# Optimization experiments

Hardware: AMD Instinct MI355X
Metric: run time of the kernel (lower is better)

Reference implementation:

```python
import jax, jax.numpy as jnp
import numpy as np
import math

H = 16          # num heads
D = 64          # head dim
MAX_POS = 512   # max_position_embeddings


def setup_inputs() -> dict:
    key = jax.random.key(0)
    ks = jax.random.split(key, 8)
    B, S, E = 8, 512, 1024
    scale = 1.0 / math.sqrt(E)
    return {
        "hidden_states": jax.random.normal(ks[0], (B, S, E), jnp.float32),
        "attention_mask": jnp.zeros((B, 1, 1, S), jnp.float32),
        "Wq": jax.random.normal(ks[1], (E, E), jnp.float32) * scale,
        "bq": jnp.zeros((E,), jnp.float32),
        "Wk": jax.random.normal(ks[2], (E, E), jnp.float32) * scale,
        "bk": jnp.zeros((E,), jnp.float32),
        "Wv": jax.random.normal(ks[3], (E, E), jnp.float32) * scale,
        "bv": jnp.zeros((E,), jnp.float32),
        "dist_emb": jax.random.normal(ks[4], (2 * MAX_POS - 1, D), jnp.float32) * 0.02,
    }


def reference(hidden_states, attention_mask, Wq, bq, Wk, bk, Wv, bv, dist_emb):
    B, S, E = hidden_states.shape

    def heads(x):  # [B,S,E] -> [B,H,S,D]
        return x.reshape(B, S, H, D).transpose(0, 2, 1, 3)

    q = heads(hidden_states @ Wq + bq)
    k = heads(hidden_states @ Wk + bk)
    v = heads(hidden_states @ Wv + bv)

    # raw scores [B,H,S,S]
    scores = jnp.einsum('bhld,bhrd->bhlr', q, k)

    # relative position embedding lookup: distance[l,r] = l - r
    pos = jnp.arange(S)
    distance = pos[:, None] - pos[None, :]               # [S,S]
    pe = dist_emb[distance + MAX_POS - 1]                # [S,S,D]
    scores = scores + jnp.einsum('bhld,lrd->bhlr', q, pe)
    scores = scores + jnp.einsum('bhrd,lrd->bhlr', k, pe)

    scores = scores / math.sqrt(D) + attention_mask
    probs = jax.nn.softmax(scores, axis=-1)

    ctx = jnp.einsum('bhlr,bhrd->bhld', probs, v)        # [B,H,S,D]
    ctx = ctx.transpose(0, 2, 1, 3).reshape(B, S, H * D)
    return ctx
```

## Files before the change

kernel.cpp:

```cpp
#include <hip/hip_runtime.h>

#define BATCH 8
#define SEQ   512
#define EMB   1024
#define NH    16
#define HD    64

typedef __bf16 bf16x8 __attribute__((ext_vector_type(8)));
typedef float  f32x4  __attribute__((ext_vector_type(4)));

__device__ __forceinline__ unsigned short f2bf(float f){
  union { float f; unsigned u; } v; v.f = f;
  unsigned r = v.u + 0x7FFFu + ((v.u >> 16) & 1u);
  return (unsigned short)(r >> 16);
}
__device__ __forceinline__ unsigned short f2bfr(float f){
  union { float f; unsigned u; } v; v.f = f;
  return (unsigned short)((v.u + 0x8000u) >> 16);
}
__device__ __forceinline__ float bf2f(unsigned short s){
  union { unsigned u; float f; } v; v.u = ((unsigned)s) << 16;
  return v.f;
}

__device__ __forceinline__ float dpp_max16(float x){
  int t;
  t = __builtin_amdgcn_update_dpp(0, __builtin_bit_cast(int, x), 0xB1, 0xF, 0xF, true);
  x = fmaxf(x, __builtin_bit_cast(float, t));
  t = __builtin_amdgcn_update_dpp(0, __builtin_bit_cast(int, x), 0x4E, 0xF, 0xF, true);
  x = fmaxf(x, __builtin_bit_cast(float, t));
  t = __builtin_amdgcn_update_dpp(0, __builtin_bit_cast(int, x), 0x141, 0xF, 0xF, true);
  x = fmaxf(x, __builtin_bit_cast(float, t));
  t = __builtin_amdgcn_update_dpp(0, __builtin_bit_cast(int, x), 0x140, 0xF, 0xF, true);
  x = fmaxf(x, __builtin_bit_cast(float, t));
  return x;
}
__device__ __forceinline__ float dpp_sum16(float x){
  int t;
  t = __builtin_amdgcn_update_dpp(0, __builtin_bit_cast(int, x), 0xB1, 0xF, 0xF, true);
  x += __builtin_bit_cast(float, t);
  t = __builtin_amdgcn_update_dpp(0, __builtin_bit_cast(int, x), 0x4E, 0xF, 0xF, true);
  x += __builtin_bit_cast(float, t);
  t = __builtin_amdgcn_update_dpp(0, __builtin_bit_cast(int, x), 0x141, 0xF, 0xF, true);
  x += __builtin_bit_cast(float, t);
  t = __builtin_amdgcn_update_dpp(0, __builtin_bit_cast(int, x), 0x140, 0xF, 0xF, true);
  x += __builtin_bit_cast(float, t);
  return x;
}

__device__ __forceinline__ int swzc(int row, int chunk){
  return row * 128 + (((chunk ^ (row & 7)) & 7) << 4);
}
__device__ __forceinline__ int swz2(int row, int col){
  return row * 128 + ((((col >> 3) ^ (row & 7)) & 7) << 4) + ((col & 7) << 1);
}

__device__ __forceinline__ void gload16(const unsigned short* g, unsigned char* lds){
  __builtin_amdgcn_global_load_lds((const __attribute__((address_space(1))) unsigned int*)g,
                                   (__attribute__((address_space(3))) unsigned int*)lds,
                                   16, 0, 0);
}

__device__ __forceinline__ void bar_lds(){
  asm volatile("s_waitcnt lgkmcnt(0)" ::: "memory");
  __builtin_amdgcn_s_barrier();
}

__global__ void k_pre(const float* __restrict__ hid, unsigned short* __restrict__ hidb,
                      const float* __restrict__ dist, unsigned short* __restrict__ distb,
                      const float* __restrict__ Wq, const float* __restrict__ Wk,
                      const float* __restrict__ Wv, unsigned short* __restrict__ wqt,
                      unsigned short* __restrict__ wkt, unsigned short* __restrict__ wvt){
  int bid = blockIdx.x;
  int t = threadIdx.x;
  if (bid < 4096){
    int i = (bid * 256 + t) * 4;
    float4 v = *(const float4*)(hid + i);
    ushort4 o; o.x = f2bf(v.x); o.y = f2bf(v.y); o.z = f2bf(v.z); o.w = f2bf(v.w);
    *(ushort4*)(hidb + i) = o;
  } else if (bid < 4352){
    int i = (bid - 4096) * 256 + t;
    distb[i] = (i < 1023 * 64) ? f2bf(dist[i]) : (unsigned short)0;
  } else {
    int wt = bid - 4352;
    int z = wt >> 10, rem = wt & 1023;
    const float* W = (z == 0) ? Wq : (z == 1) ? Wk : Wv;
    unsigned short* WT = (z == 0) ? wqt : (z == 1) ? wkt : wvt;
    __shared__ float tl[32][33];
    int n0 = (rem & 31) * 32, k0 = (rem >> 5) * 32;
    int tx = t & 31, ty = t >> 5;
#pragma unroll
    for (int i = 0; i < 4; i++)
      tl[ty + 8*i][tx] = W[(k0 + ty + 8*i) * EMB + n0 + tx];
    __syncthreads();
#pragma unroll
    for (int i = 0; i < 4; i++)
      WT[(n0 + ty + 8*i) * EMB + k0 + tx] = f2bf(tl[tx][ty + 8*i]);
  }
}

__global__ __launch_bounds__(256, 3) void k_gemm3(const unsigned short* __restrict__ A,
                                                  const unsigned short* __restrict__ wqt,
                                                  const unsigned short* __restrict__ wkt,
                                                  const unsigned short* __restrict__ wvt,
                                                  const float* __restrict__ bq,
                                                  const float* __restrict__ bk,
                                                  const float* __restrict__ bv,
                                                  unsigned short* __restrict__ qb,
                                                  unsigned short* __restrict__ kb,
                                                  unsigned short* __restrict__ vtb){
  int z = blockIdx.z;
  const unsigned short* BT = (z == 0) ? wqt : (z == 1) ? wkt : wvt;
  const float* bias = (z == 0) ? bq : (z == 1) ? bk : bv;
  unsigned short* out = (z == 0) ? qb : (z == 1) ? kb : vtb;
  int mode = (z == 2);

  __shared__ __align__(16) unsigned char sA[128 * 128];
  __shared__ __align__(16) unsigned char sB[128 * 128];
  int id2 = blockIdx.x + 8 * blockIdx.y;
  int s2  = (id2 & 7) * 32 + (id2 >> 3);
  int m0 = (s2 >> 3) * 128, n0 = (s2 & 7) * 128;
  int t = threadIdx.x, w = t >> 6, lane = t & 63, g = lane >> 4, lr = lane & 15;
  int rowbase = (w >> 1) * 64, colbase = (w & 1) * 64;
  int lrow = lane >> 3, lc = lane & 7;
  f32x4 acc[4][4] = {};
  for (int k0 = 0; k0 < EMB; k0 += 64){
    __syncthreads();
#pragma unroll
    for (int i = 0; i < 4; i++){
      int row = (w + 4*i) * 8 + lrow;
      int cg  = lc ^ (row & 7);
      gload16(A  + (m0 + row) * EMB + k0 + cg*8, sA + (w + 4*i) * 1024);
      gload16(BT + (n0 + row) * EMB + k0 + cg*8, sB + (w + 4*i) * 1024);
    }
    __syncthreads();
#pragma unroll
    for (int kk = 0; kk < 2; kk++){
      bf16x8 af[4], bfv[4];
#pragma unroll
      for (int i = 0; i < 4; i++) af[i]  = *(const bf16x8*)(sA + swzc(rowbase + 16*i + lr, kk*4 + g));
#pragma unroll
      for (int j = 0; j < 4; j++) bfv[j] = *(const bf16x8*)(sB + swzc(colbase + 16*j + lr, kk*4 + g));
#pragma unroll
      for (int i = 0; i < 4; i++)
#pragma unroll
        for (int j = 0; j < 4; j++)
          acc[i][j] = __builtin_amdgcn_mfma_f32_16x16x32_bf16(af[i], bfv[j], acc[i][j], 0, 0, 0);
    }
  }
#pragma unroll
  for (int i = 0; i < 4; i++)
#pragma unroll
    for (int j = 0; j < 4; j++)
#pragma unroll
      for (int r = 0; r < 4; r++){
        int m = m0 + rowbase + 16*i + 4*g + r;
        int n = n0 + colbase + 16*j + lr;
        float val = acc[i][j][r] + bias[n];
        int b = m >> 9, s = m & 511, h = n >> 6, d = n & 63;
        int idx = (mode == 0) ? (((b*NH + h)*SEQ + s)*HD + d)
                              : (((b*NH + h)*HD + d)*SEQ + s);
        out[idx] = f2bf(val);
      }
}

__global__ __launch_bounds__(256, 2) void k_attn(const unsigned short* __restrict__ qb,
                                                 const unsigned short* __restrict__ kb,
                                                 const unsigned short* __restrict__ vtb,
                                                 const unsigned short* __restrict__ distb,
                                                 const float* __restrict__ mask,
                                                 float* __restrict__ out){
  __shared__ __align__(16) unsigned char sK[64 * 128];
  __shared__ __align__(16) unsigned char sV[64 * 128];
  __shared__ __align__(16) unsigned char sSA[4][2624];
  __shared__ __align__(16) unsigned char sSB[4][2560];

  const float SCL  = 0.125f * 1.4426950408889634f;
  const float L2E  = 1.4426950408889634f;

  int bid = blockIdx.x;
  int wgid = (bid & 7) * 128 + (bid >> 3);
  int lt = wgid & 7, h = (wgid >> 3) & 15, b = wgid >> 7;
  int L0 = lt * 64;
  int bh = b * NH + h;
  int t = threadIdx.x, w = t >> 6, lane = t & 63, g = lane >> 4, lr = lane & 15;
  int lbase = 16 * w;
  unsigned char* mySA = sSA[w];
  unsigned char* mySB = sSB[w];
  unsigned char* myP  = mySA;
  const float* maskp = mask + b * SEQ;

  const unsigned short* qrow = qb + (bh * SEQ + L0 + lbase + lr) * HD + 8 * g;
  bf16x8 aq0 = *(const bf16x8*)qrow;
  bf16x8 aq1 = *(const bf16x8*)(qrow + 32);

  bf16x8 pe[5][2];
#define LOAD_PE(JB) do {                                                     \
    const unsigned short* _pb = distb + ((JB) + 16*w + lr) * HD + 8*g;       \
    _Pragma("unroll")                                                        \
    for (int _j = 0; _j < 5; _j++){                                          \
      pe[_j][0] = *(const bf16x8*)(_pb + _j*16*HD);                          \
      pe[_j][1] = *(const bf16x8*)(_pb + _j*16*HD + 32); }                   \
  } while(0)

  int lrow = lane >> 3, lc = lane & 7;
  int row0 = w * 8 + lrow,      row1 = (w + 4) * 8 + lrow;
  int cg0  = lc ^ (row0 & 7),   cg1  = lc ^ (row1 & 7);
  const unsigned short* kbase = kb  + bh * SEQ * HD;
  const unsigned short* vbase = vtb + bh * HD * SEQ;

  uint4 kst0 = *(const uint4*)(kbase + row0 * HD  + cg0 * 8);
  uint4 kst1 = *(const uint4*)(kbase + row1 * HD  + cg1 * 8);
  uint4 vst0 = *(const uint4*)(vbase + row0 * SEQ + cg0 * 8);
  uint4 vst1 = *(const uint4*)(vbase + row1 * SEQ + cg1 * 8);
  LOAD_PE(L0 + 448);

  f32x4 o[4] = {};
  float mrun[4], srun[4];
#pragma unroll
  for (int r = 0; r < 4; r++){ mrun[r] = -1e30f; srun[r] = 0.f; }

  for (int rt = 0; rt < 8; rt++){
    int R0 = rt * 64;

    bar_lds();

    *(uint4*)(sK + w * 1024 + lane * 16)       = kst0;
    *(uint4*)(sK + (w + 4) * 1024 + lane * 16) = kst1;
    *(uint4*)(sV + w * 1024 + lane * 16)       = vst0;
    *(uint4*)(sV + (w + 4) * 1024 + lane * 16) = vst1;

    if (rt < 7){
      const unsigned short* ks = kbase + (R0 + 64) * HD;
      const unsigned short* vs = vbase + (R0 + 64);
      kst0 = *(const uint4*)(ks + row0 * HD  + cg0 * 8);
      kst1 = *(const uint4*)(ks + row1 * HD  + cg1 * 8);
      vst0 = *(const uint4*)(vs + row0 * SEQ + cg0 * 8);
      vst1 = *(const uint4*)(vs + row1 * SEQ + cg1 * 8);
    }

    float mreg[4];
#pragma unroll
    for (int f = 0; f < 4; f++) mreg[f] = maskp[R0 + 16*f + lr];

    bar_lds();

    __builtin_amdgcn_s_setprio(1);
    f32x4 sc[4];
#pragma unroll
    for (int f = 0; f < 4; f++){
      bf16x8 k0 = *(const bf16x8*)(sK + swzc(16*f + lr, g));
      bf16x8 k1 = *(const bf16x8*)(sK + swzc(16*f + lr, 4 + g));
      f32x4 a = {};
      a = __builtin_amdgcn_mfma_f32_16x16x32_bf16(aq0, k0, a, 0, 0, 0);
      a = __builtin_amdgcn_mfma_f32_16x16x32_bf16(aq1, k1, a, 0, 0, 0);
      sc[f] = a;
      f32x4 b0 = {}, b1 = {};
      b0 = __builtin_amdgcn_mfma_f32_16x16x32_bf16(k0, pe[3 - f][0], b0, 0, 0, 0);
      b0 = __builtin_amdgcn_mfma_f32_16x16x32_bf16(k1, pe[3 - f][1], b0, 0, 0, 0);
      b1 = __builtin_amdgcn_mfma_f32_16x16x32_bf16(k0, pe[4 - f][0], b1, 0, 0, 0);
      b1 = __builtin_amdgcn_mfma_f32_16x16x32_bf16(k1, pe[4 - f][1], b1, 0, 0, 0);
#pragma unroll
      for (int reg = 0; reg < 4; reg++){
        int ss = 4*g + reg + lr;
        float v = (ss >= 15) ? b0[reg] : b1[reg];
        int row = 16*f + 4*g + reg;
        int col = (ss + 1) & 15;
        *(unsigned short*)(mySB + row*40 + col*2) = f2bfr(v);
      }
    }

#pragma unroll
    for (int jt2 = 0; jt2 < 5; jt2++){
      f32x4 a = {};
      a = __builtin_amdgcn_mfma_f32_16x16x32_bf16(aq0, pe[jt2][0], a, 0, 0, 0);
      a = __builtin_amdgcn_mfma_f32_16x16x32_bf16(aq1, pe[jt2][1], a, 0, 0, 0);
#pragma unroll
      for (int reg = 0; reg < 4; reg++){
        int rloc = 63 + 4*g + reg - lr - 16*jt2;
        int addr = ((unsigned)rloc < 64u) ? (rloc*40 + (4*g + reg)*2) : 2560;
        *(unsigned short*)(mySA + addr) = f2bfr(a[reg]);
      }
    }
    __builtin_amdgcn_s_setprio(0);

    if (rt < 7) LOAD_PE(L0 + 448 - 64*(rt + 1));

#pragma unroll
    for (int f = 0; f < 4; f++){
      ushort4 sa = *(const ushort4*)(mySA + (16*f + lr)*40 + 8*g);
      ushort4 sb = *(const ushort4*)(mySB + (16*f + lr)*40 + 8*g);
      float madd = mreg[f] * L2E;
      sc[f][0] = (sc[f][0] + bf2f(sa.x) + bf2f(sb.x)) * SCL + madd;
      sc[f][1] = (sc[f][1] + bf2f(sa.y) + bf2f(sb.y)) * SCL + madd;
      sc[f][2] = (sc[f][2] + bf2f(sa.z) + bf2f(sb.z)) * SCL + madd;
      sc[f][3] = (sc[f][3] + bf2f(sa.w) + bf2f(sb.w)) * SCL + madd;
    }

    float fac[4];
#pragma unroll
    for (int r = 0; r < 4; r++){
      float tm = fmaxf(fmaxf(sc[0][r], sc[1][r]), fmaxf(sc[2][r], sc[3][r]));
      tm = dpp_max16(tm);
      float mnew = fmaxf(mrun[r], tm);
      float fr = exp2f(mrun[r] - mnew);
      float ps = 0.f;
#pragma unroll
      for (int f = 0; f < 4; f++){ float p = exp2f(sc[f][r] - mnew); sc[f][r] = p; ps += p; }
      ps = dpp_sum16(ps);
      srun[r] = srun[r] * fr + ps;
      mrun[r] = mnew;
      fac[r]  = fr;
    }
#pragma unroll
    for (int df = 0; df < 4; df++)
#pragma unroll
      for (int r = 0; r < 4; r++) o[df][r] *= fac[r];

#pragma unroll
    for (int f = 0; f < 4; f++)
#pragma unroll
      for (int r = 0; r < 4; r++)
        *(unsigned short*)(myP + swz2(4*g + r, 16*f + lr)) = f2bfr(sc[f][r]);

    __builtin_amdgcn_s_setprio(1);
#pragma unroll
    for (int kk = 0; kk < 2; kk++){
      bf16x8 pf = *(const bf16x8*)(myP + swzc(lr, kk*4 + g));
#pragma unroll
      for (int df = 0; df < 4; df++){
        bf16x8 vf = *(const bf16x8*)(sV + swzc(16*df + lr, kk*4 + g));
        o[df] = __builtin_amdgcn_mfma_f32_16x16x32_bf16(pf, vf, o[df], 0, 0, 0);
      }
    }
    __builtin_amdgcn_s_setprio(0);
  }

#pragma unroll
  for (int r = 0; r < 4; r++){
    float inv = 1.0f / srun[r];
#pragma unroll
    for (int df = 0; df < 4; df++){
      int l = L0 + lbase + 4*g + r;
      out[(b * SEQ + l) * EMB + h * HD + 16*df + lr] = o[df][r] * inv;
    }
  }
#undef LOAD_PE
}

extern "C" void kernel_launch(void* const* d_in, const int* in_sizes, int n_in,
                              void* d_out, int out_size, void* d_ws, size_t ws_size,
                              hipStream_t stream) {
  (void)in_sizes; (void)n_in; (void)out_size; (void)ws_size;
  const float* hid  = (const float*)d_in[0];
  const float* mask = (const float*)d_in[1];
  const float* Wq   = (const float*)d_in[2];
  const float* bq   = (const float*)d_in[3];
  const float* Wk   = (const float*)d_in[4];
  const float* bk   = (const float*)d_in[5];
  const float* Wv   = (const float*)d_in[6];
  const float* bv   = (const float*)d_in[7];
  const float* dist = (const float*)d_in[8];
  float* out = (float*)d_out;

  unsigned char* ws = (unsigned char*)d_ws;
  unsigned short* hidb  = (unsigned short*)ws;
  unsigned short* wqt   = hidb + 4096 * 1024;
  unsigned short* wkt   = wqt  + 1024 * 1024;
  unsigned short* wvt   = wkt  + 1024 * 1024;
  unsigned short* distb = wvt  + 1024 * 1024;
  unsigned short* qb    = distb + 1024 * 64;
  unsigned short* kb    = qb + BATCH * NH * SEQ * HD;
  unsigned short* vtb   = kb + BATCH * NH * SEQ * HD;

  k_pre<<<7424, 256, 0, stream>>>(hid, hidb, dist, distb, Wq, Wk, Wv, wqt, wkt, wvt);
  k_gemm3<<<dim3(8, 32, 3), 256, 0, stream>>>(hidb, wqt, wkt, wvt, bq, bk, bv, qb, kb, vtb);
  k_attn<<<1024, 256, 0, stream>>>(qb, kb, vtb, distb, mask, out);
}
```

Measured before the change: 103.6 us.

## Stage two K/V tiles per barrier pair to halve attention loop synchronisation

```diff
diff --git a/kernel.cpp b/kernel.cpp
--- a/kernel.cpp
+++ b/kernel.cpp
@@ -170,8 +170,8 @@
                                                  const unsigned short* __restrict__ distb,
                                                  const float* __restrict__ mask,
                                                  float* __restrict__ out){
-  __shared__ __align__(16) unsigned char sK[64 * 128];
-  __shared__ __align__(16) unsigned char sV[64 * 128];
+  __shared__ __align__(16) unsigned char sK[2][64 * 128];
+  __shared__ __align__(16) unsigned char sV[2][64 * 128];
   __shared__ __align__(16) unsigned char sSA[4][2624];
   __shared__ __align__(16) unsigned char sSB[4][2560];
 
@@ -209,10 +209,14 @@
   const unsigned short* kbase = kb  + bh * SEQ * HD;
   const unsigned short* vbase = vtb + bh * HD * SEQ;
 
-  uint4 kst0 = *(const uint4*)(kbase + row0 * HD  + cg0 * 8);
-  uint4 kst1 = *(const uint4*)(kbase + row1 * HD  + cg1 * 8);
-  uint4 vst0 = *(const uint4*)(vbase + row0 * SEQ + cg0 * 8);
-  uint4 vst1 = *(const uint4*)(vbase + row1 * SEQ + cg1 * 8);
+  uint4 k0a = *(const uint4*)(kbase + row0 * HD  + cg0 * 8);
+  uint4 k0b = *(const uint4*)(kbase + row1 * HD  + cg1 * 8);
+  uint4 v0a = *(const uint4*)(vbase + row0 * SEQ + cg0 * 8);
+  uint4 v0b = *(const uint4*)(vbase + row1 * SEQ + cg1 * 8);
+  uint4 k1a = *(const uint4*)(kbase + 64 * HD + row0 * HD  + cg0 * 8);
+  uint4 k1b = *(const uint4*)(kbase + 64 * HD + row1 * HD  + cg1 * 8);
+  uint4 v1a = *(const uint4*)(vbase + 64      + row0 * SEQ + cg0 * 8);
+  uint4 v1b = *(const uint4*)(vbase + 64      + row1 * SEQ + cg1 * 8);
   LOAD_PE(L0 + 448);
 
   f32x4 o[4] = {};
@@ -220,120 +224,134 @@
 #pragma unroll
   for (int r = 0; r < 4; r++){ mrun[r] = -1e30f; srun[r] = 0.f; }
 
-  for (int rt = 0; rt < 8; rt++){
-    int R0 = rt * 64;
-
+  for (int s = 0; s < 4; s++){
     bar_lds();
 
-    *(uint4*)(sK + w * 1024 + lane * 16)       = kst0;
-    *(uint4*)(sK + (w + 4) * 1024 + lane * 16) = kst1;
-    *(uint4*)(sV + w * 1024 + lane * 16)       = vst0;
-    *(uint4*)(sV + (w + 4) * 1024 + lane * 16) = vst1;
-
-    if (rt < 7){
-      const unsigned short* ks = kbase + (R0 + 64) * HD;
-      const unsigned short* vs = vbase + (R0 + 64);
-      kst0 = *(const uint4*)(ks + row0 * HD  + cg0 * 8);
-      kst1 = *(const uint4*)(ks + row1 * HD  + cg1 * 8);
-      vst0 = *(const uint4*)(vs + row0 * SEQ + cg0 * 8);
-      vst1 = *(const uint4*)(vs + row1 * SEQ + cg1 * 8);
-    }
-
-    float mreg[4];
-#pragma unroll
-    for (int f = 0; f < 4; f++) mreg[f] = maskp[R0 + 16*f + lr];
+    *(uint4*)(sK[0] + w * 1024 + lane * 16)       = k0a;
+    *(uint4*)(sK[0] + (w + 4) * 1024 + lane * 16) = k0b;
+    *(uint4*)(sV[0] + w * 1024 + lane * 16)       = v0a;
+    *(uint4*)(sV[0] + (w + 4) * 1024 + lane * 16) = v0b;
+    *(uint4*)(sK[1] + w * 1024 + lane * 16)       = k1a;
+    *(uint4*)(sK[1] + (w + 4) * 1024 + lane * 16) = k1b;
+    *(uint4*)(sV[1] + w * 1024 + lane * 16)       = v1a;
+    *(uint4*)(sV[1] + (w + 4) * 1024 + lane * 16) = v1b;
+
+    if (s < 3){
+      const unsigned short* ks = kbase + (s * 128 + 128) * HD;
+      const unsigned short* vs = vbase + (s * 128 + 128);
+      k0a = *(const uint4*)(ks + row0 * HD  + cg0 * 8);
+      k0b = *(const uint4*)(ks + row1 * HD  + cg1 * 8);
+      v0a = *(const uint4*)(vs + row0 * SEQ + cg0 * 8);
+      v0b = *(const uint4*)(vs + row1 * SEQ + cg1 * 8);
+      k1a = *(const uint4*)(ks + 64 * HD + row0 * HD  + cg0 * 8);
+      k1b = *(const uint4*)(ks + 64 * HD + row1 * HD  + cg1 * 8);
+      v1a = *(const uint4*)(vs + 64      + row0 * SEQ + cg0 * 8);
+      v1b = *(const uint4*)(vs + 64      + row1 * SEQ + cg1 * 8);
+    }
 
     bar_lds();
 
-    __builtin_amdgcn_s_setprio(1);
-    f32x4 sc[4];
-#pragma unroll
-    for (int f = 0; f < 4; f++){
-      bf16x8 k0 = *(const bf16x8*)(sK + swzc(16*f + lr, g));
-      bf16x8 k1 = *(const bf16x8*)(sK + swzc(16*f + lr, 4 + g));
-      f32x4 a = {};
-      a = __builtin_amdgcn_mfma_f32_16x16x32_bf16(aq0, k0, a, 0, 0, 0);
-      a = __builtin_amdgcn_mfma_f32_16x16x32_bf16(aq1, k1, a, 0, 0, 0);
-      sc[f] = a;
-      f32x4 b0 = {}, b1 = {};
-      b0 = __builtin_amdgcn_mfma_f32_16x16x32_bf16(k0, pe[3 - f][0], b0, 0, 0, 0);
-      b0 = __builtin_amdgcn_mfma_f32_16x16x32_bf16(k1, pe[3 - f][1], b0, 0, 0, 0);
-      b1 = __builtin_amdgcn_mfma_f32_16x16x32_bf16(k0, pe[4 - f][0], b1, 0, 0, 0);
-      b1 = __builtin_amdgcn_mfma_f32_16x16x32_bf16(k1, pe[4 - f][1], b1, 0, 0, 0);
-#pragma unroll
-      for (int reg = 0; reg < 4; reg++){
-        int ss = 4*g + reg + lr;
-        float v = (ss >= 15) ? b0[reg] : b1[reg];
-        int row = 16*f + 4*g + reg;
-        int col = (ss + 1) & 15;
-        *(unsigned short*)(mySB + row*40 + col*2) = f2bfr(v);
-      }
-    }
-
-#pragma unroll
-    for (int jt2 = 0; jt2 < 5; jt2++){
-      f32x4 a = {};
-      a = __builtin_amdgcn_mfma_f32_16x16x32_bf16(aq0, pe[jt2][0], a, 0, 0, 0);
-      a = __builtin_amdgcn_mfma_f32_16x16x32_bf16(aq1, pe[jt2][1], a, 0, 0, 0);
-#pragma unroll
-      for (int reg = 0; reg < 4; reg++){
-        int rloc = 63 + 4*g + reg - lr - 16*jt2;
-        int addr = ((unsigned)rloc < 64u) ? (rloc*40 + (4*g + reg)*2) : 2560;
-        *(unsigned short*)(mySA + addr) = f2bfr(a[reg]);
-      }
-    }
-    __builtin_amdgcn_s_setprio(0);
-
-    if (rt < 7) LOAD_PE(L0 + 448 - 64*(rt + 1));
-
-#pragma unroll
-    for (int f = 0; f < 4; f++){
-      ushort4 sa = *(const ushort4*)(mySA + (16*f + lr)*40 + 8*g);
-      ushort4 sb = *(const ushort4*)(mySB + (16*f + lr)*40 + 8*g);
-      float madd = mreg[f] * L2E;
-      sc[f][0] = (sc[f][0] + bf2f(sa.x) + bf2f(sb.x)) * SCL + madd;
-      sc[f][1] = (sc[f][1] + bf2f(sa.y) + bf2f(sb.y)) * SCL + madd;
-      sc[f][2] = (sc[f][2] + bf2f(sa.z) + bf2f(sb.z)) * SCL + madd;
-      sc[f][3] = (sc[f][3] + bf2f(sa.w) + bf2f(sb.w)) * SCL + madd;
-    }
-
-    float fac[4];
-#pragma unroll
-    for (int r = 0; r < 4; r++){
-      float tm = fmaxf(fmaxf(sc[0][r], sc[1][r]), fmaxf(sc[2][r], sc[3][r]));
-      tm = dpp_max16(tm);
-      float mnew = fmaxf(mrun[r], tm);
-      float fr = exp2f(mrun[r] - mnew);
-      float ps = 0.f;
-#pragma unroll
-      for (int f = 0; f < 4; f++){ float p = exp2f(sc[f][r] - mnew); sc[f][r] = p; ps += p; }
-      ps = dpp_sum16(ps);
-      srun[r] = srun[r] * fr + ps;
-      mrun[r] = mnew;
-      fac[r]  = fr;
-    }
-#pragma unroll
-    for (int df = 0; df < 4; df++)
-#pragma unroll
-      for (int r = 0; r < 4; r++) o[df][r] *= fac[r];
-
-#pragma unroll
-    for (int f = 0; f < 4; f++)
-#pragma unroll
-      for (int r = 0; r < 4; r++)
-        *(unsigned short*)(myP + swz2(4*g + r, 16*f + lr)) = f2bfr(sc[f][r]);
-
-    __builtin_amdgcn_s_setprio(1);
-#pragma unroll
-    for (int kk = 0; kk < 2; kk++){
-      bf16x8 pf = *(const bf16x8*)(myP + swzc(lr, kk*4 + g));
-#pragma unroll
-      for (int df = 0; df < 4; df++){
-        bf16x8 vf = *(const bf16x8*)(sV + swzc(16*df + lr, kk*4 + g));
-        o[df] = __builtin_amdgcn_mfma_f32_16x16x32_bf16(pf, vf, o[df], 0, 0, 0);
-      }
-    }
-    __builtin_amdgcn_s_setprio(0);
+#pragma unroll
+    for (int half = 0; half < 2; half++){
+      int rt = 2 * s + half;
+      int R0 = rt * 64;
+      const unsigned char* sKh = sK[half];
+      const unsigned char* sVh = sV[half];
+
+      float mreg[4];
+#pragma unroll
+      for (int f = 0; f < 4; f++) mreg[f] = maskp[R0 + 16*f + lr];
+
+      __builtin_amdgcn_s_setprio(1);
+      f32x4 sc[4];
+#pragma unroll
+      for (int f = 0; f < 4; f++){
+        bf16x8 k0 = *(const bf16x8*)(sKh + swzc(16*f + lr, g));
+        bf16x8 k1 = *(const bf16x8*)(sKh + swzc(16*f + lr, 4 + g));
+        f32x4 a = {};
+        a = __builtin_amdgcn_mfma_f32_16x16x32_bf16(aq0, k0, a, 0, 0, 0);
+        a = __builtin_amdgcn_mfma_f32_16x16x32_bf16(aq1, k1, a, 0, 0, 0);
+        sc[f] = a;
+        f32x4 b0 = {}, b1 = {};
+        b0 = __builtin_amdgcn_mfma_f32_16x16x32_bf16(k0, pe[3 - f][0], b0, 0, 0, 0);
+        b0 = __builtin_amdgcn_mfma_f32_16x16x32_bf16(k1, pe[3 - f][1], b0, 0, 0, 0);
+        b1 = __builtin_amdgcn_mfma_f32_16x16x32_bf16(k0, pe[4 - f][0], b1, 0, 0, 0);
+        b1 = __builtin_amdgcn_mfma_f32_16x16x32_bf16(k1, pe[4 - f][1], b1, 0, 0, 0);
+#pragma unroll
+        for (int reg = 0; reg < 4; reg++){
+          int ss = 4*g + reg + lr;
+          float v = (ss >= 15) ? b0[reg] : b1[reg];
+          int row = 16*f + 4*g + reg;
+          int col = (ss + 1) & 15;
+          *(unsigned short*)(mySB + row*40 + col*2) = f2bfr(v);
+        }
+      }
+
+#pragma unroll
+      for (int jt2 = 0; jt2 < 5; jt2++){
+        f32x4 a = {};
+        a = __builtin_amdgcn_mfma_f32_16x16x32_bf16(aq0, pe[jt2][0], a, 0, 0, 0);
+        a = __builtin_amdgcn_mfma_f32_16x16x32_bf16(aq1, pe[jt2][1], a, 0, 0, 0);
+#pragma unroll
+        for (int reg = 0; reg < 4; reg++){
+          int rloc = 63 + 4*g + reg - lr - 16*jt2;
+          int addr = ((unsigned)rloc < 64u) ? (rloc*40 + (4*g + reg)*2) : 2560;
+          *(unsigned short*)(mySA + addr) = f2bfr(a[reg]);
+        }
+      }
+      __builtin_amdgcn_s_setprio(0);
+
+      if (rt < 7) LOAD_PE(L0 + 448 - 64*(rt + 1));
+
+#pragma unroll
+      for (int f = 0; f < 4; f++){
+        ushort4 sa = *(const ushort4*)(mySA + (16*f + lr)*40 + 8*g);
+        ushort4 sb = *(const ushort4*)(mySB + (16*f + lr)*40 + 8*g);
+        float madd = mreg[f] * L2E;
+        sc[f][0] = (sc[f][0] + bf2f(sa.x) + bf2f(sb.x)) * SCL + madd;
+        sc[f][1] = (sc[f][1] + bf2f(sa.y) + bf2f(sb.y)) * SCL + madd;
+        sc[f][2] = (sc[f][2] + bf2f(sa.z) + bf2f(sb.z)) * SCL + madd;
+        sc[f][3] = (sc[f][3] + bf2f(sa.w) + bf2f(sb.w)) * SCL + madd;
+      }
+
+      float fac[4];
+#pragma unroll
+      for (int r = 0; r < 4; r++){
+        float tm = fmaxf(fmaxf(sc[0][r], sc[1][r]), fmaxf(sc[2][r], sc[3][r]));
+        tm = dpp_max16(tm);
+        float mnew = fmaxf(mrun[r], tm);
+        float fr = exp2f(mrun[r] - mnew);
+        float ps = 0.f;
+#pragma unroll
+        for (int f = 0; f < 4; f++){ float p = exp2f(sc[f][r] - mnew); sc[f][r] = p; ps += p; }
+        ps = dpp_sum16(ps);
+        srun[r] = srun[r] * fr + ps;
+        mrun[r] = mnew;
+        fac[r]  = fr;
+      }
+#pragma unroll
+      for (int df = 0; df < 4; df++)
+#pragma unroll
+        for (int r = 0; r < 4; r++) o[df][r] *= fac[r];
+
+#pragma unroll
+      for (int f = 0; f < 4; f++)
+#pragma unroll
+        for (int r = 0; r < 4; r++)
+          *(unsigned short*)(myP + swz2(4*g + r, 16*f + lr)) = f2bfr(sc[f][r]);
+
+      __builtin_amdgcn_s_setprio(1);
+#pragma unroll
+      for (int kk = 0; kk < 2; kk++){
+        bf16x8 pf = *(const bf16x8*)(myP + swzc(lr, kk*4 + g));
+#pragma unroll
+        for (int df = 0; df < 4; df++){
+          bf16x8 vf = *(const bf16x8*)(sVh + swzc(16*df + lr, kk*4 + g));
+          o[df] = __builtin_amdgcn_mfma_f32_16x16x32_bf16(pf, vf, o[df], 0, 0, 0);
+        }
+      }
+      __builtin_amdgcn_s_setprio(0);
+    }
   }
 
 #pragma unroll
```

Result: slower. 112.5 us (+8.5%).

## Load K and V tiles directly from global memory, dropping shared staging and barriers

Applied to the files above, without the earlier changes.

```diff
diff --git a/kernel.cpp b/kernel.cpp
--- a/kernel.cpp
+++ b/kernel.cpp
@@ -59,11 +59,6 @@
   __builtin_amdgcn_global_load_lds((const __attribute__((address_space(1))) unsigned int*)g,
                                    (__attribute__((address_space(3))) unsigned int*)lds,
                                    16, 0, 0);
-}
-
-__device__ __forceinline__ void bar_lds(){
-  asm volatile("s_waitcnt lgkmcnt(0)" ::: "memory");
-  __builtin_amdgcn_s_barrier();
 }
 
 __global__ void k_pre(const float* __restrict__ hid, unsigned short* __restrict__ hidb,
@@ -170,10 +165,9 @@
                                                  const unsigned short* __restrict__ distb,
                                                  const float* __restrict__ mask,
                                                  float* __restrict__ out){
-  __shared__ __align__(16) unsigned char sK[64 * 128];
-  __shared__ __align__(16) unsigned char sV[64 * 128];
   __shared__ __align__(16) unsigned char sSA[4][2624];
   __shared__ __align__(16) unsigned char sSB[4][2560];
+  __shared__ __align__(16) unsigned char sP[4][2048];
 
   const float SCL  = 0.125f * 1.4426950408889634f;
   const float L2E  = 1.4426950408889634f;
@@ -187,7 +181,7 @@
   int lbase = 16 * w;
   unsigned char* mySA = sSA[w];
   unsigned char* mySB = sSB[w];
-  unsigned char* myP  = mySA;
+  unsigned char* myP  = sP[w];
   const float* maskp = mask + b * SEQ;
 
   const unsigned short* qrow = qb + (bh * SEQ + L0 + lbase + lr) * HD + 8 * g;
@@ -203,16 +197,9 @@
       pe[_j][1] = *(const bf16x8*)(_pb + _j*16*HD + 32); }                   \
   } while(0)
 
-  int lrow = lane >> 3, lc = lane & 7;
-  int row0 = w * 8 + lrow,      row1 = (w + 4) * 8 + lrow;
-  int cg0  = lc ^ (row0 & 7),   cg1  = lc ^ (row1 & 7);
   const unsigned short* kbase = kb  + bh * SEQ * HD;
   const unsigned short* vbase = vtb + bh * HD * SEQ;
 
-  uint4 kst0 = *(const uint4*)(kbase + row0 * HD  + cg0 * 8);
-  uint4 kst1 = *(const uint4*)(kbase + row1 * HD  + cg1 * 8);
-  uint4 vst0 = *(const uint4*)(vbase + row0 * SEQ + cg0 * 8);
-  uint4 vst1 = *(const uint4*)(vbase + row1 * SEQ + cg1 * 8);
   LOAD_PE(L0 + 448);
 
   f32x4 o[4] = {};
@@ -222,35 +209,26 @@
 
   for (int rt = 0; rt < 8; rt++){
     int R0 = rt * 64;
-
-    bar_lds();
-
-    *(uint4*)(sK + w * 1024 + lane * 16)       = kst0;
-    *(uint4*)(sK + (w + 4) * 1024 + lane * 16) = kst1;
-    *(uint4*)(sV + w * 1024 + lane * 16)       = vst0;
-    *(uint4*)(sV + (w + 4) * 1024 + lane * 16) = vst1;
-
-    if (rt < 7){
-      const unsigned short* ks = kbase + (R0 + 64) * HD;
-      const unsigned short* vs = vbase + (R0 + 64);
-      kst0 = *(const uint4*)(ks + row0 * HD  + cg0 * 8);
-      kst1 = *(const uint4*)(ks + row1 * HD  + cg1 * 8);
-      vst0 = *(const uint4*)(vs + row0 * SEQ + cg0 * 8);
-      vst1 = *(const uint4*)(vs + row1 * SEQ + cg1 * 8);
-    }
+    const unsigned short* kt = kbase + R0 * HD;
+    const unsigned short* vt = vbase + R0;
+
+    bf16x8 vf[2][4];
+#pragma unroll
+    for (int kk = 0; kk < 2; kk++)
+#pragma unroll
+      for (int df = 0; df < 4; df++)
+        vf[kk][df] = *(const bf16x8*)(vt + (16*df + lr) * SEQ + kk*32 + 8*g);
 
     float mreg[4];
 #pragma unroll
     for (int f = 0; f < 4; f++) mreg[f] = maskp[R0 + 16*f + lr];
-
-    bar_lds();
 
     __builtin_amdgcn_s_setprio(1);
     f32x4 sc[4];
 #pragma unroll
     for (int f = 0; f < 4; f++){
-      bf16x8 k0 = *(const bf16x8*)(sK + swzc(16*f + lr, g));
-      bf16x8 k1 = *(const bf16x8*)(sK + swzc(16*f + lr, 4 + g));
+      bf16x8 k0 = *(const bf16x8*)(kt + (16*f + lr) * HD + 8*g);
+      bf16x8 k1 = *(const bf16x8*)(kt + (16*f + lr) * HD + 32 + 8*g);
       f32x4 a = {};
       a = __builtin_amdgcn_mfma_f32_16x16x32_bf16(aq0, k0, a, 0, 0, 0);
       a = __builtin_amdgcn_mfma_f32_16x16x32_bf16(aq1, k1, a, 0, 0, 0);
@@ -328,10 +306,8 @@
     for (int kk = 0; kk < 2; kk++){
       bf16x8 pf = *(const bf16x8*)(myP + swzc(lr, kk*4 + g));
 #pragma unroll
-      for (int df = 0; df < 4; df++){
-        bf16x8 vf = *(const bf16x8*)(sV + swzc(16*df + lr, kk*4 + g));
-        o[df] = __builtin_amdgcn_mfma_f32_16x16x32_bf16(pf, vf, o[df], 0, 0, 0);
-      }
+      for (int df = 0; df < 4; df++)
+        o[df] = __builtin_amdgcn_mfma_f32_16x16x32_bf16(pf, vf[kk][df], o[df], 0, 0, 0);
     }
     __builtin_amdgcn_s_setprio(0);
   }
```

New measurement: 146.0 us. 1.41x slower.
